# Kernel optimization log

Hardware: AMD Instinct MI355X
Metric: run time of the kernel (lower is better)

## Reference

```python
import jax, jax.numpy as jnp
import numpy as np

DIM = 512
HEADS = 8
HEAD_DIM = DIM // HEADS
SCALE = HEAD_DIM ** -0.5


def setup_inputs() -> dict:
    key = jax.random.key(0)
    ks = jax.random.split(key, 7)
    B, QN, N = 32, 128, 4096
    q = jax.random.normal(ks[0], (B, QN, DIM), dtype=jnp.float32)
    kv = jax.random.normal(ks[1], (B, N, DIM), dtype=jnp.float32)
    key_mask = jax.random.normal(ks[2], (B, QN, N), dtype=jnp.float32)
    Wq = jax.random.normal(ks[3], (DIM, DIM), dtype=jnp.float32) * 0.02
    Wkv = jax.random.normal(ks[4], (2 * DIM, DIM), dtype=jnp.float32) * 0.02
    Wproj = jax.random.normal(ks[5], (DIM, DIM), dtype=jnp.float32) * 0.02
    bproj = jax.random.normal(ks[6], (DIM,), dtype=jnp.float32) * 0.02
    return {"q": q, "kv": kv, "key_mask": key_mask,
            "Wq": Wq, "Wkv": Wkv, "Wproj": Wproj, "bproj": bproj}


def reference(q, kv, key_mask, Wq, Wkv, Wproj, bproj):
    B, QN, C = q.shape
    N = kv.shape[1]
    # q projection -> [B, QN, H, hd]
    qh = (q @ Wq.T).reshape(B, QN, HEADS, HEAD_DIM) * SCALE
    # kv projection -> split into k, v each [B, N, H, hd]
    kvp = kv @ Wkv.T  # [B, N, 2C]
    k = kvp[..., :C].reshape(B, N, HEADS, HEAD_DIM)
    v = kvp[..., C:].reshape(B, N, HEADS, HEAD_DIM)
    # scores [B, H, QN, N] + additive mask broadcast over heads
    attn = jnp.einsum('bqhd,bkhd->bhqk', qh, k) + key_mask[:, None]
    attn = jax.nn.softmax(attn, axis=-1)
    x = jnp.einsum('bhqk,bkhd->bqhd', attn, v).reshape(B, QN, C)
    return x @ Wproj.T + bproj
```

## Files before the change

### kernel.cpp

```cpp
#include <hip/hip_runtime.h>
#include <hip/hip_bf16.h>

typedef __attribute__((ext_vector_type(4))) float f32x4;
typedef __attribute__((ext_vector_type(8))) short bf16x8;

#define GAS __attribute__((address_space(1)))
#define LAS __attribute__((address_space(3)))

__device__ __forceinline__ unsigned int cvtpk(float lo, float hi) {
  unsigned int r;
  asm("v_cvt_pk_bf16_f32 %0, %1, %2" : "=v"(r) : "v"(lo), "v"(hi));
  return r;
}
__device__ __forceinline__ unsigned short f2bf(float f) { return (unsigned short)cvtpk(f, f); }
__device__ __forceinline__ f32x4 mfma16(bf16x8 a, bf16x8 b, f32x4 c) {
  return __builtin_amdgcn_mfma_f32_16x16x32_bf16(a, b, c, 0, 0, 0);
}
__device__ __forceinline__ void gl_lds16(const unsigned short* g, unsigned short* l) {
  __builtin_amdgcn_global_load_lds((const GAS unsigned short*)g, (LAS unsigned short*)l, 16, 0, 0);
}
__device__ __forceinline__ void memfence_sched() { asm volatile("" ::: "memory"); }

__global__ __launch_bounds__(256)
void cvt_f32_bf16(const float* __restrict__ in, unsigned short* __restrict__ out, int n8) {
  for (int i = blockIdx.x * blockDim.x + threadIdx.x; i < n8; i += gridDim.x * blockDim.x) {
    const float4 a = *reinterpret_cast<const float4*>(in + (size_t)i * 8);
    const float4 b = *reinterpret_cast<const float4*>(in + (size_t)i * 8 + 4);
    uint4 o;
    o.x = cvtpk(a.x, a.y); o.y = cvtpk(a.z, a.w);
    o.z = cvtpk(b.x, b.y); o.w = cvtpk(b.z, b.w);
    *reinterpret_cast<uint4*>(out + (size_t)i * 8) = o;
  }
}

template<int MODE>
__global__ __launch_bounds__(512, 2)
void gemm8p(const unsigned short* __restrict__ Ag, const unsigned short* __restrict__ Bg,
            void* __restrict__ Cg, const float* __restrict__ bias, int ntn, size_t ldc)
{
  __shared__ unsigned short sm[49152];
  const int t = threadIdx.x, lane = t & 63, w = t >> 6;
  const int lo = lane & 15, hi = lane >> 4;
  const int wm = w >> 2, wn = w & 3;
  const int nwg = gridDim.x, bid = blockIdx.x;
  const int id = (bid & 7) * (nwg >> 3) + (bid >> 3);
  const int row0 = (id / ntn) * 256, col0 = (id % ntn) * 256;

  const int gcol = ((t & 3) * 8) ^ (((t >> 5) & 1) << 4);
  const int grow = t >> 2;
  const unsigned short* aS = Ag + (size_t)(row0 + grow) * 512 + gcol;
  const unsigned short* bS = Bg + (size_t)(col0 + grow) * 512 + gcol;
  const int wds = w * 512;

  auto STAGE_A = [&](int kt) {
    const int bf = kt % 3;
    gl_lds16(aS + kt * 32,         &sm[(bf * 2 + 0) * 4096 + wds]);
    gl_lds16(aS + kt * 32 + 65536, &sm[(bf * 2 + 1) * 4096 + wds]);
  };
  auto STAGE_B = [&](int kt) {
    const int bf = kt % 3;
    gl_lds16(bS + kt * 32,         &sm[24576 + (bf * 2 + 0) * 4096 + wds]);
    gl_lds16(bS + kt * 32 + 65536, &sm[24576 + (bf * 2 + 1) * 4096 + wds]);
  };

  f32x4 acc[8][4] = {};
  const int fc = (hi * 8) ^ (((lo >> 3) & 1) << 4);
  const int rbB = (wn & 1) * 64;

  STAGE_A(0); STAGE_B(0); STAGE_A(1); STAGE_B(1);
  memfence_sched();
  asm volatile("s_waitcnt vmcnt(4)" ::: "memory");
  __builtin_amdgcn_s_barrier();
  memfence_sched();

  #pragma unroll
  for (int kt = 0; kt < 16; ++kt) {
    const int bf = kt % 3;
    const unsigned short* aB = &sm[(bf * 2 + wm) * 4096];
    const unsigned short* bB = &sm[24576 + (bf * 2 + (wn >> 1)) * 4096];

    bf16x8 bfr[4], af[4];
    #pragma unroll
    for (int nj = 0; nj < 4; ++nj)
      bfr[nj] = *reinterpret_cast<const bf16x8*>(&bB[(rbB + nj * 16 + lo) * 32 + fc]);
    #pragma unroll
    for (int mi = 0; mi < 4; ++mi)
      af[mi] = *reinterpret_cast<const bf16x8*>(&aB[(mi * 16 + lo) * 32 + fc]);
    if (kt <= 13) STAGE_A(kt + 2);
    memfence_sched();
    __builtin_amdgcn_s_barrier();
    memfence_sched();
    __builtin_amdgcn_s_setprio(1);
    #pragma unroll
    for (int mi = 0; mi < 4; ++mi)
      #pragma unroll
      for (int nj = 0; nj < 4; ++nj)
        acc[mi][nj] = mfma16(af[mi], bfr[nj], acc[mi][nj]);
    __builtin_amdgcn_s_setprio(0);
    __builtin_amdgcn_s_barrier();
    memfence_sched();

    #pragma unroll
    for (int mi = 0; mi < 4; ++mi)
      af[mi] = *reinterpret_cast<const bf16x8*>(&aB[((mi + 4) * 16 + lo) * 32 + fc]);
    if (kt <= 13) STAGE_B(kt + 2);
    memfence_sched();
    __builtin_amdgcn_s_barrier();
    memfence_sched();
    __builtin_amdgcn_s_setprio(1);
    #pragma unroll
    for (int mi = 0; mi < 4; ++mi)
      #pragma unroll
      for (int nj = 0; nj < 4; ++nj)
        acc[mi + 4][nj] = mfma16(af[mi], bfr[nj], acc[mi + 4][nj]);
    __builtin_amdgcn_s_setprio(0);
    if (kt <= 13)      { asm volatile("s_waitcnt vmcnt(4)" ::: "memory"); }
    else if (kt == 14) { asm volatile("s_waitcnt vmcnt(0)" ::: "memory"); }
    if (kt < 15) { __builtin_amdgcn_s_barrier(); memfence_sched(); }
  }

  #pragma unroll
  for (int mi = 0; mi < 8; ++mi) {
    #pragma unroll
    for (int r = 0; r < 4; ++r) {
      const size_t gm = (size_t)row0 + wm * 128 + mi * 16 + hi * 4 + r;
      #pragma unroll
      for (int nj = 0; nj < 4; ++nj) {
        const int gn = col0 + wn * 64 + nj * 16 + lo;
        const float v = acc[mi][nj][r];
        if constexpr (MODE == 0)
          ((unsigned short*)Cg)[gm * ldc + gn] = f2bf(v * 0.125f);
        else if constexpr (MODE == 1)
          ((unsigned short*)Cg)[gm * ldc + gn] = f2bf(v);
        else
          ((float*)Cg)[gm * ldc + gn] = v + bias[gn];
      }
    }
  }
}

__global__ __launch_bounds__(256)
void attn_fwd(const unsigned short* __restrict__ qh,
              const unsigned short* __restrict__ kbuf,
              const unsigned short* __restrict__ vT,
              const float* __restrict__ mask,
              float* __restrict__ opart, float* __restrict__ ml)
{
  __shared__ unsigned short Ks[64 * 64];
  __shared__ unsigned short Vs[64 * 64];
  __shared__ unsigned short Ps[4][16 * 64];
  const int bid = blockIdx.x;
  const int xcd = bid & 7, g = bid >> 3;
  const int b = (g >> 6) * 8 + xcd;
  const int sub = g & 63;
  const int h = sub >> 3, qhalf = (sub >> 2) & 1, c = sub & 3;
  const int n0 = c * 1024;
  const int bh2 = (b * 8 + h) * 2 + qhalf;
  const int t = threadIdx.x, lane = t & 63, w = t >> 6;
  const int hi = lane >> 4, lo = lane & 15;
  const int q0 = qhalf * 64 + w * 16;

  bf16x8 aq[2];
  #pragma unroll
  for (int kk = 0; kk < 2; ++kk)
    aq[kk] = *reinterpret_cast<const bf16x8*>(
        qh + (size_t)(b * 128 + q0 + lo) * 512 + h * 64 + kk * 32 + hi * 8);

  float mrow[4], lrow[4];
  #pragma unroll
  for (int i = 0; i < 4; ++i) { mrow[i] = -1e30f; lrow[i] = 0.f; }
  f32x4 o[4] = {};

  const unsigned short* kp = kbuf + ((size_t)b * 4096 + n0) * 512 + h * 64;
  const unsigned short* vp = vT + (size_t)(h * 64) * 131072 + (size_t)b * 4096 + n0;
  const float* mp = mask + ((size_t)(b * 128 + q0)) * 4096 + n0;

  for (int nt = 0; nt < 16; ++nt) {
    {
      const int r = t >> 3, cc = t & 7;
      *reinterpret_cast<uint4*>(&Ks[r * 64 + ((cc ^ (r & 7)) << 3)]) =
          *reinterpret_cast<const uint4*>(kp + (size_t)(nt * 64 + r) * 512 + (cc << 3));
      *reinterpret_cast<uint4*>(&Ks[(r + 32) * 64 + ((cc ^ (r & 7)) << 3)]) =
          *reinterpret_cast<const uint4*>(kp + (size_t)(nt * 64 + r + 32) * 512 + (cc << 3));
      *reinterpret_cast<uint4*>(&Vs[r * 64 + ((cc ^ (r & 7)) << 3)]) =
          *reinterpret_cast<const uint4*>(vp + (size_t)r * 131072 + nt * 64 + (cc << 3));
      *reinterpret_cast<uint4*>(&Vs[(r + 32) * 64 + ((cc ^ (r & 7)) << 3)]) =
          *reinterpret_cast<const uint4*>(vp + (size_t)(r + 32) * 131072 + nt * 64 + (cc << 3));
    }
    __syncthreads();

    f32x4 s[4] = {};
    __builtin_amdgcn_s_setprio(1);
    #pragma unroll
    for (int ni = 0; ni < 4; ++ni) {
      #pragma unroll
      for (int kk = 0; kk < 2; ++kk) {
        const bf16x8 kf = *reinterpret_cast<const bf16x8*>(
            &Ks[(ni * 16 + lo) * 64 + ((kk * 32 + hi * 8) ^ ((lo & 7) << 3))]);
        s[ni] = mfma16(aq[kk], kf, s[ni]);
      }
    }
    __builtin_amdgcn_s_setprio(0);
    #pragma unroll
    for (int ni = 0; ni < 4; ++ni)
      #pragma unroll
      for (int r = 0; r < 4; ++r)
        s[ni][r] += mp[(size_t)(hi * 4 + r) * 4096 + nt * 64 + ni * 16 + lo];

    #pragma unroll
    for (int r = 0; r < 4; ++r) {
      float mx = fmaxf(fmaxf(s[0][r], s[1][r]), fmaxf(s[2][r], s[3][r]));
      #pragma unroll
      for (int off = 1; off < 16; off <<= 1)
        mx = fmaxf(mx, __shfl_xor(mx, off, 64));
      const float mnew = fmaxf(mrow[r], mx);
      const float corr = __expf(mrow[r] - mnew);
      mrow[r] = mnew;
      float ls = 0.f;
      #pragma unroll
      for (int ni = 0; ni < 4; ++ni) {
        const float p = __expf(s[ni][r] - mnew);
        s[ni][r] = p; ls += p;
      }
      #pragma unroll
      for (int off = 1; off < 16; off <<= 1)
        ls += __shfl_xor(ls, off, 64);
      lrow[r] = lrow[r] * corr + ls;
      #pragma unroll
      for (int di = 0; di < 4; ++di)
        o[di][r] *= corr;
    }

    #pragma unroll
    for (int ni = 0; ni < 4; ++ni)
      #pragma unroll
      for (int r = 0; r < 4; ++r) {
        const int rp = hi * 4 + r;
        Ps[w][rp * 64 + ((ni * 16 + lo) ^ ((rp & 7) << 3))] = f2bf(s[ni][r]);
      }

    __builtin_amdgcn_s_setprio(1);
    #pragma unroll
    for (int kk = 0; kk < 2; ++kk) {
      const bf16x8 pa = *reinterpret_cast<const bf16x8*>(
          &Ps[w][lo * 64 + ((kk * 32 + hi * 8) ^ ((lo & 7) << 3))]);
      #pragma unroll
      for (int di = 0; di < 4; ++di) {
        const bf16x8 vf = *reinterpret_cast<const bf16x8*>(
            &Vs[(di * 16 + lo) * 64 + ((kk * 32 + hi * 8) ^ ((lo & 7) << 3))]);
        o[di] = mfma16(pa, vf, o[di]);
      }
    }
    __builtin_amdgcn_s_setprio(0);
    __syncthreads();
  }

  const size_t pbase = ((size_t)bh2 * 4 + c) * 64;
  #pragma unroll
  for (int di = 0; di < 4; ++di)
    #pragma unroll
    for (int r = 0; r < 4; ++r)
      opart[(pbase + (w * 16 + hi * 4 + r)) * 64 + di * 16 + lo] = o[di][r];
  if (lo == 0) {
    #pragma unroll
    for (int r = 0; r < 4; ++r) {
      const int qq = w * 16 + hi * 4 + r;
      ml[(((size_t)bh2 * 4 + c) * 2 + 0) * 64 + qq] = mrow[r];
      ml[(((size_t)bh2 * 4 + c) * 2 + 1) * 64 + qq] = lrow[r];
    }
  }
}

__global__ __launch_bounds__(256)
void attn_combine(const float* __restrict__ opart, const float* __restrict__ ml,
                  unsigned short* __restrict__ xb)
{
  const int bh2 = blockIdx.x;
  const int b = bh2 >> 4, h = (bh2 >> 1) & 7, qhalf = bh2 & 1;
  const int t = threadIdx.x;
  const int q = t >> 2, dg = t & 3;

  float m[4], l[4];
  #pragma unroll
  for (int c = 0; c < 4; ++c) {
    m[c] = ml[(((size_t)bh2 * 4 + c) * 2 + 0) * 64 + q];
    l[c] = ml[(((size_t)bh2 * 4 + c) * 2 + 1) * 64 + q];
  }
  const float M = fmaxf(fmaxf(m[0], m[1]), fmaxf(m[2], m[3]));
  float sc[4], L = 0.f;
  #pragma unroll
  for (int c = 0; c < 4; ++c) { sc[c] = __expf(m[c] - M); L += sc[c] * l[c]; }
  const float inv = 1.f / L;

  float4 acc[4] = {};
  #pragma unroll
  for (int c = 0; c < 4; ++c) {
    const float* base = opart + (((size_t)bh2 * 4 + c) * 64 + q) * 64 + dg * 16;
    #pragma unroll
    for (int j = 0; j < 4; ++j) {
      const float4 v = *reinterpret_cast<const float4*>(base + j * 4);
      acc[j].x = fmaf(sc[c], v.x, acc[j].x);
      acc[j].y = fmaf(sc[c], v.y, acc[j].y);
      acc[j].z = fmaf(sc[c], v.z, acc[j].z);
      acc[j].w = fmaf(sc[c], v.w, acc[j].w);
    }
  }
  unsigned short* dst = xb + ((size_t)b * 128 + qhalf * 64 + q) * 512 + h * 64 + dg * 16;
  uint4 o1, o2;
  o1.x = cvtpk(acc[0].x * inv, acc[0].y * inv); o1.y = cvtpk(acc[0].z * inv, acc[0].w * inv);
  o1.z = cvtpk(acc[1].x * inv, acc[1].y * inv); o1.w = cvtpk(acc[1].z * inv, acc[1].w * inv);
  o2.x = cvtpk(acc[2].x * inv, acc[2].y * inv); o2.y = cvtpk(acc[2].z * inv, acc[2].w * inv);
  o2.z = cvtpk(acc[3].x * inv, acc[3].y * inv); o2.w = cvtpk(acc[3].z * inv, acc[3].w * inv);
  *reinterpret_cast<uint4*>(dst) = o1;
  *reinterpret_cast<uint4*>(dst + 8) = o2;
}

extern "C" void kernel_launch(void* const* d_in, const int* in_sizes, int n_in,
                              void* d_out, int out_size, void* d_ws, size_t ws_size,
                              hipStream_t stream) {
  const float* q     = (const float*)d_in[0];
  const float* kv    = (const float*)d_in[1];
  const float* mask  = (const float*)d_in[2];
  const float* Wq    = (const float*)d_in[3];
  const float* Wkv   = (const float*)d_in[4];
  const float* Wproj = (const float*)d_in[5];
  const float* bproj = (const float*)d_in[6];
  float* out = (float*)d_out;

  char* ws = (char*)d_ws;
  unsigned short* kbuf   = (unsigned short*)ws;
  unsigned short* vTb    = (unsigned short*)(ws + 134217728ULL);
  unsigned short* kvbfc  = (unsigned short*)(ws + 268435456ULL);
  unsigned short* qbf    = kvbfc;
  float*          opart  = (float*)(ws + 268435456ULL);
  float*          mlb    = (float*)(ws + 301989888ULL);
  unsigned short* xb     = (unsigned short*)(ws + 303038464ULL);
  unsigned short* qhb    = (unsigned short*)(ws + 335544320ULL);
  unsigned short* Wqb    = (unsigned short*)(ws + 339738624ULL);
  unsigned short* Wkvb   = (unsigned short*)(ws + 340262912ULL);
  unsigned short* Wprojb = (unsigned short*)(ws + 341311488ULL);

  cvt_f32_bf16<<<128, 256, 0, stream>>>(Wq, Wqb, 512 * 512 / 8);
  cvt_f32_bf16<<<256, 256, 0, stream>>>(Wkv, Wkvb, 1024 * 512 / 8);
  cvt_f32_bf16<<<128, 256, 0, stream>>>(Wproj, Wprojb, 512 * 512 / 8);

  cvt_f32_bf16<<<256, 256, 0, stream>>>(q, qbf, 4096 * 512 / 8);
  gemm8p<0><<<32, 512, 0, stream>>>(qbf, Wqb, qhb, nullptr, 2, 512);

  for (int c = 0; c < 2; ++c) {
    cvt_f32_bf16<<<2048, 256, 0, stream>>>(kv + (size_t)c * 65536 * 512, kvbfc,
                                           65536 * 512 / 8);
    gemm8p<1><<<512, 512, 0, stream>>>(kvbfc, Wkvb,
                                       kbuf + (size_t)c * 65536 * 512, nullptr, 2, 512);
    gemm8p<1><<<512, 512, 0, stream>>>(Wkvb + 512 * 512, kvbfc,
                                       vTb + (size_t)c * 65536, nullptr, 256, 131072);
  }

  attn_fwd<<<2048, 256, 0, stream>>>(qhb, kbuf, vTb, mask, opart, mlb);
  attn_combine<<<512, 256, 0, stream>>>(opart, mlb, xb);
  gemm8p<2><<<32, 512, 0, stream>>>(xb, Wprojb, out, bproj, 2, 512);
}
```

Measured before the change: 439.7 us.

## Deepen GEMM LDS pipeline to four stages with new swizzle, one block per CU

The 8-wave GEMM goes from a triple-buffered to a quad-buffered LDS ring: it prefetches three k-tiles ahead instead of two and adjusts the vmcnt waits to match. It also changes the LDS layout to a contiguous 256-row block per operand with an XOR swizzle keyed on the row's low bits, and each wave indexes rows by its wm/wn offset. LDS use grows to 128KB, so the launch bound drops to one block per CU. Deeper prefetch should hide more global-load latency, at the cost of losing the second resident block that could overlap one block's epilogue with another's main loop.

```diff
diff --git a/kernel.cpp b/kernel.cpp
--- a/kernel.cpp
+++ b/kernel.cpp
@@ -34,11 +34,11 @@
 }
 
 template<int MODE>
-__global__ __launch_bounds__(512, 2)
+__global__ __launch_bounds__(512, 1)
 void gemm8p(const unsigned short* __restrict__ Ag, const unsigned short* __restrict__ Bg,
             void* __restrict__ Cg, const float* __restrict__ bias, int ntn, size_t ldc)
 {
-  __shared__ unsigned short sm[49152];
+  __shared__ unsigned short sm[65536];
   const int t = threadIdx.x, lane = t & 63, w = t >> 6;
   const int lo = lane & 15, hi = lane >> 4;
   const int wm = w >> 2, wn = w & 3;
@@ -46,47 +46,45 @@
   const int id = (bid & 7) * (nwg >> 3) + (bid >> 3);
   const int row0 = (id / ntn) * 256, col0 = (id % ntn) * 256;
 
-  const int gcol = ((t & 3) * 8) ^ (((t >> 5) & 1) << 4);
-  const int grow = t >> 2;
-  const unsigned short* aS = Ag + (size_t)(row0 + grow) * 512 + gcol;
-  const unsigned short* bS = Bg + (size_t)(col0 + grow) * 512 + gcol;
-  const int wds = w * 512;
+  const int srow = t >> 2;
+  const int scol = ((t & 3) * 8) ^ ((srow & 3) << 3);
+  const unsigned short* aS = Ag + (size_t)(row0 + srow) * 512 + scol;
+  const unsigned short* bS = Bg + (size_t)(col0 + srow) * 512 + scol;
+  const int wbase = w * 512;
 
   auto STAGE_A = [&](int kt) {
-    const int bf = kt % 3;
-    gl_lds16(aS + kt * 32,         &sm[(bf * 2 + 0) * 4096 + wds]);
-    gl_lds16(aS + kt * 32 + 65536, &sm[(bf * 2 + 1) * 4096 + wds]);
+    const int bf = kt & 3;
+    gl_lds16(aS + kt * 32,         &sm[bf * 8192 + wbase]);
+    gl_lds16(aS + kt * 32 + 65536, &sm[bf * 8192 + 4096 + wbase]);
   };
   auto STAGE_B = [&](int kt) {
-    const int bf = kt % 3;
-    gl_lds16(bS + kt * 32,         &sm[24576 + (bf * 2 + 0) * 4096 + wds]);
-    gl_lds16(bS + kt * 32 + 65536, &sm[24576 + (bf * 2 + 1) * 4096 + wds]);
+    const int bf = kt & 3;
+    gl_lds16(bS + kt * 32,         &sm[32768 + bf * 8192 + wbase]);
+    gl_lds16(bS + kt * 32 + 65536, &sm[32768 + bf * 8192 + 4096 + wbase]);
   };
 
   f32x4 acc[8][4] = {};
-  const int fc = (hi * 8) ^ (((lo >> 3) & 1) << 4);
-  const int rbB = (wn & 1) * 64;
-
-  STAGE_A(0); STAGE_B(0); STAGE_A(1); STAGE_B(1);
+  const int fc = (hi * 8) ^ ((lo & 3) << 3);
+
+  STAGE_A(0); STAGE_B(0); STAGE_A(1); STAGE_B(1); STAGE_A(2); STAGE_B(2);
   memfence_sched();
-  asm volatile("s_waitcnt vmcnt(4)" ::: "memory");
+  asm volatile("s_waitcnt vmcnt(8)" ::: "memory");
   __builtin_amdgcn_s_barrier();
   memfence_sched();
 
   #pragma unroll
   for (int kt = 0; kt < 16; ++kt) {
-    const int bf = kt % 3;
-    const unsigned short* aB = &sm[(bf * 2 + wm) * 4096];
-    const unsigned short* bB = &sm[24576 + (bf * 2 + (wn >> 1)) * 4096];
+    const unsigned short* aB = &sm[(kt & 3) * 8192];
+    const unsigned short* bB = &sm[32768 + (kt & 3) * 8192];
 
     bf16x8 bfr[4], af[4];
     #pragma unroll
     for (int nj = 0; nj < 4; ++nj)
-      bfr[nj] = *reinterpret_cast<const bf16x8*>(&bB[(rbB + nj * 16 + lo) * 32 + fc]);
+      bfr[nj] = *reinterpret_cast<const bf16x8*>(&bB[(wn * 64 + nj * 16 + lo) * 32 + fc]);
     #pragma unroll
     for (int mi = 0; mi < 4; ++mi)
-      af[mi] = *reinterpret_cast<const bf16x8*>(&aB[(mi * 16 + lo) * 32 + fc]);
-    if (kt <= 13) STAGE_A(kt + 2);
+      af[mi] = *reinterpret_cast<const bf16x8*>(&aB[(wm * 128 + mi * 16 + lo) * 32 + fc]);
+    if (kt <= 12) STAGE_A(kt + 3);
     memfence_sched();
     __builtin_amdgcn_s_barrier();
     memfence_sched();
@@ -102,8 +100,8 @@
 
     #pragma unroll
     for (int mi = 0; mi < 4; ++mi)
-      af[mi] = *reinterpret_cast<const bf16x8*>(&aB[((mi + 4) * 16 + lo) * 32 + fc]);
-    if (kt <= 13) STAGE_B(kt + 2);
+      af[mi] = *reinterpret_cast<const bf16x8*>(&aB[((wm * 128) + (mi + 4) * 16 + lo) * 32 + fc]);
+    if (kt <= 12) STAGE_B(kt + 3);
     memfence_sched();
     __builtin_amdgcn_s_barrier();
     memfence_sched();
@@ -114,7 +112,8 @@
       for (int nj = 0; nj < 4; ++nj)
         acc[mi + 4][nj] = mfma16(af[mi], bfr[nj], acc[mi + 4][nj]);
     __builtin_amdgcn_s_setprio(0);
-    if (kt <= 13)      { asm volatile("s_waitcnt vmcnt(4)" ::: "memory"); }
+    if (kt <= 12)      { asm volatile("s_waitcnt vmcnt(8)" ::: "memory"); }
+    else if (kt == 13) { asm volatile("s_waitcnt vmcnt(4)" ::: "memory"); }
     else if (kt == 14) { asm volatile("s_waitcnt vmcnt(0)" ::: "memory"); }
     if (kt < 15) { __builtin_amdgcn_s_barrier(); memfence_sched(); }
   }
```

Result: slower. 449.6 us (+2.3%).
